# Optimization experiments

Measured on AMD Instinct MI355X. Metric: run time of the kernel, lower is better.

Reference implementation:

```python
import jax, jax.numpy as jnp
import numpy as np

N_HEAD = 16
N_FEAT = 1024
D_K = N_FEAT // N_HEAD  # 64
BLOCK_SIZE = 32
MAX_BLOCKS = 512
CHUNK = 1024
OFFSET = 3072  # cache_seqlens[0]: frames already committed to the cache
SCALE = 0.02


def setup_inputs() -> dict:
    key = jax.random.key(0)
    ks = jax.random.split(key, 12)
    # logical -> physical block mapping: a fixed permutation (irregular access)
    rng = np.random.default_rng(0)
    block_table = jnp.asarray(rng.permutation(MAX_BLOCKS).astype(np.int32))[None, :]
    return {
        "x": jax.random.normal(ks[0], (1, CHUNK, N_FEAT), jnp.float32),
        "Wq": jax.random.normal(ks[1], (N_FEAT, N_FEAT), jnp.float32) * SCALE,
        "bq": jax.random.normal(ks[2], (N_FEAT,), jnp.float32) * SCALE,
        "Wk": jax.random.normal(ks[3], (N_FEAT, N_FEAT), jnp.float32) * SCALE,
        "bk": jax.random.normal(ks[4], (N_FEAT,), jnp.float32) * SCALE,
        "Wv": jax.random.normal(ks[5], (N_FEAT, N_FEAT), jnp.float32) * SCALE,
        "bv": jax.random.normal(ks[6], (N_FEAT,), jnp.float32) * SCALE,
        "Wo": jax.random.normal(ks[7], (N_FEAT, N_FEAT), jnp.float32) * SCALE,
        "bo": jax.random.normal(ks[8], (N_FEAT,), jnp.float32) * SCALE,
        "k_cache": jax.random.normal(ks[9], (MAX_BLOCKS, BLOCK_SIZE, N_HEAD, D_K), jnp.float32),
        "v_cache": jax.random.normal(ks[10], (MAX_BLOCKS, BLOCK_SIZE, N_HEAD, D_K), jnp.float32),
        "block_table": block_table,
        "seqlen_offset": OFFSET,
    }


def reference(x, Wq, bq, Wk, bk, Wv, bv, Wo, bo, k_cache, v_cache, block_table, seqlen_offset):
    B, T, _ = x.shape  # B == 1 (streaming decode)
    # forward_qkv: Q/K/V projections, split into heads
    q = (x @ Wq + bq).reshape(B, T, N_HEAD, D_K).transpose(0, 2, 1, 3)  # (1,h,T,d)
    k_new = (x @ Wk + bk).reshape(B, T, N_HEAD, D_K)                    # (1,T,h,d)
    v_new = (x @ Wv + bv).reshape(B, T, N_HEAD, D_K)

    # _paged_write_kv: scatter the chunk frames into the physical block pool
    pos = seqlen_offset + jnp.arange(T)              # absolute frame indices
    phys = block_table[0, pos // BLOCK_SIZE]         # physical block per frame
    off = pos % BLOCK_SIZE                           # offset within block
    k_cache = k_cache.at[phys, off].set(k_new[0])
    v_cache = v_cache.at[phys, off].set(v_new[0])

    # _paged_gather_kv: gather all total_frames (old + just-written) frames
    total = seqlen_offset + T
    nblk = (total + BLOCK_SIZE - 1) // BLOCK_SIZE
    bids = block_table[0, :nblk]
    kf = k_cache[bids].reshape(-1, N_HEAD, D_K)[:total]  # (total, h, d)
    vf = v_cache[bids].reshape(-1, N_HEAD, D_K)[:total]

    # SDPA over the gathered K/V (no mask; softmax in fp32 as in the source)
    scores = jnp.einsum('bhqd,khd->bhqk', q, kf) / np.float32(np.sqrt(D_K))
    attn = jax.nn.softmax(scores.astype(jnp.float32), axis=-1).astype(x.dtype)
    ctx = jnp.einsum('bhqk,khd->bhqd', attn, vf)         # (1,h,T,d)

    # forward_attention tail: merge heads + output projection
    out = ctx.transpose(0, 2, 1, 3).reshape(B, T, N_HEAD * D_K) @ Wo + bo
    return out
```

## Files before the change

kernel.cpp:

```cpp
#include <hip/hip_runtime.h>
#include <hip/hip_bf16.h>

#define NFEAT 1024
#define NHEAD 16
#define DK 64
#define TCHUNK 1024
#define MAXTOK 4096
#define NSPLIT 4

using bf16x8 = __attribute__((ext_vector_type(8))) short;
using f32x4  = __attribute__((ext_vector_type(4))) float;

__device__ __forceinline__ short f2bf(float f) {
    __hip_bfloat16 h = __float2bfloat16(f);
    return *reinterpret_cast<short*>(&h);
}

__device__ __forceinline__ float exp2fast(float x) {
    return __builtin_amdgcn_exp2f(x);
}

#define QSCALE 0.1803368801f

__global__ __launch_bounds__(256) void pack_kernel(
    const float* __restrict__ x,
    const float* __restrict__ Wq, const float* __restrict__ Wk,
    const float* __restrict__ Wv, const float* __restrict__ Wo,
    short* __restrict__ xb, short* __restrict__ Wt) {
    const int b = blockIdx.x;
    const int t = threadIdx.x;
    if (b < 1024) {
        __shared__ short T[64][72];
        const int w = b >> 8, tile = b & 255;
        const int k0 = (tile >> 4) << 6, n0 = (tile & 15) << 6;
        const float* W = (w == 0) ? Wq : (w == 1) ? Wk : (w == 2) ? Wv : Wo;
        const int r = t >> 2, cs = (t & 3) << 4;
        #pragma unroll
        for (int u = 0; u < 4; ++u) {
            float4 v = *reinterpret_cast<const float4*>(
                &W[(size_t)(k0 + r) * NFEAT + n0 + cs + u * 4]);
            T[cs + u * 4 + 0][r] = f2bf(v.x);
            T[cs + u * 4 + 1][r] = f2bf(v.y);
            T[cs + u * 4 + 2][r] = f2bf(v.z);
            T[cs + u * 4 + 3][r] = f2bf(v.w);
        }
        __syncthreads();
        const int c = t >> 2, rs = (t & 3) << 4;
        bf16x8 a0 = *reinterpret_cast<const bf16x8*>(&T[c][rs]);
        bf16x8 a1 = *reinterpret_cast<const bf16x8*>(&T[c][rs + 8]);
        size_t drow = (size_t)(w * 1024 + n0 + c) * NFEAT + k0 + rs;
        *reinterpret_cast<bf16x8*>(&Wt[drow]) = a0;
        *reinterpret_cast<bf16x8*>(&Wt[drow + 8]) = a1;
    } else {
        const int e0 = ((b - 1024) * 256 + t) * 32;
        #pragma unroll
        for (int u = 0; u < 4; ++u) {
            float4 v0 = *reinterpret_cast<const float4*>(&x[e0 + u * 8]);
            float4 v1 = *reinterpret_cast<const float4*>(&x[e0 + u * 8 + 4]);
            bf16x8 o;
            o[0] = f2bf(v0.x); o[1] = f2bf(v0.y); o[2] = f2bf(v0.z); o[3] = f2bf(v0.w);
            o[4] = f2bf(v1.x); o[5] = f2bf(v1.y); o[6] = f2bf(v1.z); o[7] = f2bf(v1.w);
            *reinterpret_cast<bf16x8*>(&xb[e0 + u * 8]) = o;
        }
    }
}

__global__ __launch_bounds__(256) void qkv_gemm(
    const short* __restrict__ xb, const short* __restrict__ Wt,
    const float* __restrict__ bq, const float* __restrict__ bk,
    const float* __restrict__ bv, short* __restrict__ qkvb) {
    __shared__ short As[64][72];
    __shared__ short Bs[128][72];
    const int tid = threadIdx.x;
    const int lane = tid & 63;
    const int w = tid >> 6;
    const int l15 = lane & 15, lg = lane >> 4;
    const int wr = w >> 1, wc = w & 1;
    const int m0 = blockIdx.y << 6, n0 = blockIdx.x << 7;
    const int sel = n0 >> 10;
    const float* bias = (sel == 0) ? bq : (sel == 1) ? bk : bv;
    const float oscale = (sel == 0) ? QSCALE : 1.0f;

    f32x4 acc[2][4];
    #pragma unroll
    for (int i = 0; i < 2; ++i)
        #pragma unroll
        for (int j = 0; j < 4; ++j) acc[i][j] = (f32x4){0.f, 0.f, 0.f, 0.f};

    for (int k0 = 0; k0 < NFEAT; k0 += 64) {
        #pragma unroll
        for (int r = 0; r < 2; ++r) {
            int f = tid + (r << 8);
            int row = f >> 3, kc = (f & 7) << 3;
            *reinterpret_cast<bf16x8*>(&As[row][kc]) =
                *reinterpret_cast<const bf16x8*>(&xb[(size_t)(m0 + row) * NFEAT + k0 + kc]);
        }
        #pragma unroll
        for (int r = 0; r < 4; ++r) {
            int f = tid + (r << 8);
            int row = f >> 3, kc = (f & 7) << 3;
            *reinterpret_cast<bf16x8*>(&Bs[row][kc]) =
                *reinterpret_cast<const bf16x8*>(&Wt[(size_t)(n0 + row) * NFEAT + k0 + kc]);
        }
        __syncthreads();
        #pragma unroll
        for (int kk = 0; kk < 2; ++kk) {
            bf16x8 am[2], bn[4];
            #pragma unroll
            for (int mi = 0; mi < 2; ++mi)
                am[mi] = *reinterpret_cast<const bf16x8*>(
                    &As[wr * 32 + mi * 16 + l15][kk * 32 + lg * 8]);
            #pragma unroll
            for (int ni = 0; ni < 4; ++ni)
                bn[ni] = *reinterpret_cast<const bf16x8*>(
                    &Bs[wc * 64 + ni * 16 + l15][kk * 32 + lg * 8]);
            #pragma unroll
            for (int mi = 0; mi < 2; ++mi)
                #pragma unroll
                for (int ni = 0; ni < 4; ++ni)
                    acc[mi][ni] = __builtin_amdgcn_mfma_f32_16x16x32_bf16(
                        am[mi], bn[ni], acc[mi][ni], 0, 0, 0);
        }
        __syncthreads();
    }
    #pragma unroll
    for (int mi = 0; mi < 2; ++mi)
        #pragma unroll
        for (int rr = 0; rr < 4; ++rr) {
            int m = m0 + wr * 32 + mi * 16 + lg * 4 + rr;
            #pragma unroll
            for (int ni = 0; ni < 4; ++ni) {
                int n = n0 + wc * 64 + ni * 16 + l15;
                float v = (acc[mi][ni][rr] + bias[n & 1023]) * oscale;
                qkvb[(size_t)m * 3072 + n] = f2bf(v);
            }
        }
}

__global__ __launch_bounds__(256) void out_gemm(
    const short* __restrict__ ctxb, const short* __restrict__ Wt,
    const float* __restrict__ bo, float* __restrict__ out) {
    __shared__ short As[64][72];
    __shared__ short Bs[64][72];
    const int tid = threadIdx.x;
    const int lane = tid & 63;
    const int w = tid >> 6;
    const int l15 = lane & 15, lg = lane >> 4;
    const int wr = w >> 1, wc = w & 1;
    const int m0 = blockIdx.y << 6, n0 = blockIdx.x << 6;

    f32x4 acc[2][2];
    #pragma unroll
    for (int i = 0; i < 2; ++i)
        #pragma unroll
        for (int j = 0; j < 2; ++j) acc[i][j] = (f32x4){0.f, 0.f, 0.f, 0.f};

    for (int k0 = 0; k0 < NFEAT; k0 += 64) {
        #pragma unroll
        for (int r = 0; r < 2; ++r) {
            int f = tid + (r << 8);
            int row = f >> 3, kc = (f & 7) << 3;
            *reinterpret_cast<bf16x8*>(&As[row][kc]) =
                *reinterpret_cast<const bf16x8*>(&ctxb[(size_t)(m0 + row) * NFEAT + k0 + kc]);
            *reinterpret_cast<bf16x8*>(&Bs[row][kc]) =
                *reinterpret_cast<const bf16x8*>(
                    &Wt[(size_t)(3072 + n0 + row) * NFEAT + k0 + kc]);
        }
        __syncthreads();
        #pragma unroll
        for (int kk = 0; kk < 2; ++kk) {
            bf16x8 am[2], bn[2];
            #pragma unroll
            for (int mi = 0; mi < 2; ++mi)
                am[mi] = *reinterpret_cast<const bf16x8*>(
                    &As[wr * 32 + mi * 16 + l15][kk * 32 + lg * 8]);
            #pragma unroll
            for (int ni = 0; ni < 2; ++ni)
                bn[ni] = *reinterpret_cast<const bf16x8*>(
                    &Bs[wc * 32 + ni * 16 + l15][kk * 32 + lg * 8]);
            #pragma unroll
            for (int mi = 0; mi < 2; ++mi)
                #pragma unroll
                for (int ni = 0; ni < 2; ++ni)
                    acc[mi][ni] = __builtin_amdgcn_mfma_f32_16x16x32_bf16(
                        am[mi], bn[ni], acc[mi][ni], 0, 0, 0);
        }
        __syncthreads();
    }
    #pragma unroll
    for (int mi = 0; mi < 2; ++mi)
        #pragma unroll
        for (int rr = 0; rr < 4; ++rr) {
            int m = m0 + wr * 32 + mi * 16 + lg * 4 + rr;
            #pragma unroll
            for (int ni = 0; ni < 2; ++ni) {
                int n = n0 + wc * 32 + ni * 16 + l15;
                out[(size_t)m * NFEAT + n] = acc[mi][ni][rr] + bo[n];
            }
        }
}

__global__ __launch_bounds__(256) void gather_kv(
    const float* __restrict__ kc, const float* __restrict__ vc,
    const short* __restrict__ qkvb, const int* __restrict__ btab,
    const int* __restrict__ soff, short* __restrict__ kg, short* __restrict__ vt) {
    __shared__ short TV[64][72];
    const int h = blockIdx.x;
    const int t0 = blockIdx.y << 6;
    const int offset = soff[0], total = offset + TCHUNK;
    const int t = threadIdx.x;
    const int row = t >> 2, ds = (t & 3) << 4;
    const int tok = t0 + row;
    short kv[16], vv[16];
    if (tok < offset) {
        int phys = btab[tok >> 5];
        size_t base = ((size_t)(phys * 32 + (tok & 31)) * NHEAD + h) * DK + ds;
        #pragma unroll
        for (int u = 0; u < 4; ++u) {
            float4 kf = *reinterpret_cast<const float4*>(&kc[base + u * 4]);
            float4 vf = *reinterpret_cast<const float4*>(&vc[base + u * 4]);
            kv[u * 4 + 0] = f2bf(kf.x); kv[u * 4 + 1] = f2bf(kf.y);
            kv[u * 4 + 2] = f2bf(kf.z); kv[u * 4 + 3] = f2bf(kf.w);
            vv[u * 4 + 0] = f2bf(vf.x); vv[u * 4 + 1] = f2bf(vf.y);
            vv[u * 4 + 2] = f2bf(vf.z); vv[u * 4 + 3] = f2bf(vf.w);
        }
    } else if (tok < total) {
        size_t base = (size_t)(tok - offset) * 3072 + 1024 + h * DK + ds;
        bf16x8 k0 = *reinterpret_cast<const bf16x8*>(&qkvb[base]);
        bf16x8 k1 = *reinterpret_cast<const bf16x8*>(&qkvb[base + 8]);
        bf16x8 v0 = *reinterpret_cast<const bf16x8*>(&qkvb[base + 1024]);
        bf16x8 v1 = *reinterpret_cast<const bf16x8*>(&qkvb[base + 1032]);
        #pragma unroll
        for (int e = 0; e < 8; ++e) {
            kv[e] = k0[e]; kv[8 + e] = k1[e];
            vv[e] = v0[e]; vv[8 + e] = v1[e];
        }
    } else {
        #pragma unroll
        for (int e = 0; e < 16; ++e) { kv[e] = 0; vv[e] = 0; }
    }
    {
        bf16x8 a, b;
        #pragma unroll
        for (int e = 0; e < 8; ++e) { a[e] = kv[e]; b[e] = kv[8 + e]; }
        size_t kb = ((size_t)h * MAXTOK + tok) * DK + ds;
        *reinterpret_cast<bf16x8*>(&kg[kb]) = a;
        *reinterpret_cast<bf16x8*>(&kg[kb + 8]) = b;
    }
    #pragma unroll
    for (int e = 0; e < 16; ++e) TV[ds + e][row] = vv[e];
    __syncthreads();
    {
        const int d = t >> 2, ts = (t & 3) << 4;
        bf16x8 a = *reinterpret_cast<const bf16x8*>(&TV[d][ts]);
        bf16x8 b = *reinterpret_cast<const bf16x8*>(&TV[d][ts + 8]);
        size_t vb = ((size_t)h * DK + d) * MAXTOK + t0 + ts;
        *reinterpret_cast<bf16x8*>(&vt[vb]) = a;
        *reinterpret_cast<bf16x8*>(&vt[vb + 8]) = b;
    }
}

__global__ __launch_bounds__(256, 4) void attn_mfma(
    const short* __restrict__ qkvb, const short* __restrict__ kg,
    const short* __restrict__ vt, const int* __restrict__ soff,
    float* __restrict__ pacc) {
    __shared__ short Ks[64][72];
    __shared__ short Vs[64][72];
    __shared__ short Ps[4][16][72];

    const int tid = threadIdx.x;
    const int lane = tid & 63;
    const int w = tid >> 6;
    const int l15 = lane & 15;
    const int lg = lane >> 4;
    const int h = blockIdx.x;
    const int qt = blockIdx.y;
    const int z = blockIdx.z;
    const int offset = soff[0];
    const int total = offset + TCHUNK;
    const int ntiles = (total + 63) >> 6;
    const int NT = (ntiles + NSPLIT - 1) / NSPLIT;
    const int tbase = z * NT;
    const int tend = min(tbase + NT, ntiles);

    const int srow = tid >> 2;
    const int sds = (tid & 3) << 4;

    const short* kbase = kg + (size_t)h * MAXTOK * DK;
    const short* vbase = vt + (size_t)h * DK * MAXTOK;

    const size_t qrow = (size_t)(qt * 64 + w * 16 + l15) * 3072 + h * DK;
    bf16x8 aq0 = *reinterpret_cast<const bf16x8*>(&qkvb[qrow + lg * 8]);
    bf16x8 aq1 = *reinterpret_cast<const bf16x8*>(&qkvb[qrow + 32 + lg * 8]);

    bf16x8 ones;
    #pragma unroll
    for (int e = 0; e < 8; ++e) ones[e] = (short)0x3F80;

    float m[4];
    f32x4 acc[4], acc1;
    #pragma unroll
    for (int r = 0; r < 4; ++r) m[r] = -1e30f;
    #pragma unroll
    for (int fc = 0; fc < 4; ++fc) acc[fc] = (f32x4){0.f, 0.f, 0.f, 0.f};
    acc1 = (f32x4){0.f, 0.f, 0.f, 0.f};

    bf16x8 kr0, kr1, vr0, vr1;
    if (tbase < tend) {
        int tok0 = tbase << 6;
        size_t kb = (size_t)(tok0 + srow) * DK + sds;
        kr0 = *reinterpret_cast<const bf16x8*>(&kbase[kb]);
        kr1 = *reinterpret_cast<const bf16x8*>(&kbase[kb + 8]);
        size_t vb = (size_t)srow * MAXTOK + tok0 + sds;
        vr0 = *reinterpret_cast<const bf16x8*>(&vbase[vb]);
        vr1 = *reinterpret_cast<const bf16x8*>(&vbase[vb + 8]);
    }

    for (int t = tbase; t < tend; ++t) {
        __syncthreads();
        *reinterpret_cast<bf16x8*>(&Ks[srow][sds]) = kr0;
        *reinterpret_cast<bf16x8*>(&Ks[srow][sds + 8]) = kr1;
        *reinterpret_cast<bf16x8*>(&Vs[srow][sds]) = vr0;
        *reinterpret_cast<bf16x8*>(&Vs[srow][sds + 8]) = vr1;
        __syncthreads();
        if (t + 1 < tend) {
            int tok0 = (t + 1) << 6;
            size_t kb = (size_t)(tok0 + srow) * DK + sds;
            kr0 = *reinterpret_cast<const bf16x8*>(&kbase[kb]);
            kr1 = *reinterpret_cast<const bf16x8*>(&kbase[kb + 8]);
            size_t vb = (size_t)srow * MAXTOK + tok0 + sds;
            vr0 = *reinterpret_cast<const bf16x8*>(&vbase[vb]);
            vr1 = *reinterpret_cast<const bf16x8*>(&vbase[vb + 8]);
        }

        const int kt0 = t << 6;
        bf16x8 kb0[4], kb1[4];
        #pragma unroll
        for (int fc = 0; fc < 4; ++fc) {
            kb0[fc] = *reinterpret_cast<const bf16x8*>(&Ks[fc * 16 + l15][lg * 8]);
            kb1[fc] = *reinterpret_cast<const bf16x8*>(&Ks[fc * 16 + l15][32 + lg * 8]);
        }
        f32x4 s[4];
        __builtin_amdgcn_s_setprio(1);
        #pragma unroll
        for (int fc = 0; fc < 4; ++fc) {
            s[fc] = __builtin_amdgcn_mfma_f32_16x16x32_bf16(
                aq0, kb0[fc], (f32x4){0.f, 0.f, 0.f, 0.f}, 0, 0, 0);
            s[fc] = __builtin_amdgcn_mfma_f32_16x16x32_bf16(
                aq1, kb1[fc], s[fc], 0, 0, 0);
        }
        __builtin_amdgcn_s_setprio(0);
        if (kt0 + 64 > total) {
            #pragma unroll
            for (int fc = 0; fc < 4; ++fc) {
                bool valid = (kt0 + fc * 16 + l15) < total;
                #pragma unroll
                for (int r = 0; r < 4; ++r)
                    s[fc][r] = valid ? s[fc][r] : -1e30f;
            }
        }
        float lm[4];
        #pragma unroll
        for (int r = 0; r < 4; ++r)
            lm[r] = fmaxf(fmaxf(s[0][r], s[1][r]), fmaxf(s[2][r], s[3][r]));
        bool ok = lm[0] <= m[0] + 8.f && lm[1] <= m[1] + 8.f &&
                  lm[2] <= m[2] + 8.f && lm[3] <= m[3] + 8.f;
        if (!__all(ok)) {
            #pragma unroll
            for (int r = 0; r < 4; ++r) {
                float tm = lm[r];
                tm = fmaxf(tm, __shfl_xor(tm, 1));
                tm = fmaxf(tm, __shfl_xor(tm, 2));
                tm = fmaxf(tm, __shfl_xor(tm, 4));
                tm = fmaxf(tm, __shfl_xor(tm, 8));
                float mn = fmaxf(m[r], tm);
                float sc = exp2fast(m[r] - mn);
                m[r] = mn;
                acc1[r] *= sc;
                #pragma unroll
                for (int fc = 0; fc < 4; ++fc) acc[fc][r] *= sc;
            }
        }
        #pragma unroll
        for (int fc = 0; fc < 4; ++fc)
            #pragma unroll
            for (int r = 0; r < 4; ++r)
                Ps[w][lg * 4 + r][l15 + 16 * fc] = f2bf(exp2fast(s[fc][r] - m[r]));
        #pragma unroll
        for (int ks = 0; ks < 2; ++ks) {
            bf16x8 pa = *reinterpret_cast<const bf16x8*>(
                &Ps[w][l15][ks * 32 + lg * 8]);
            __builtin_amdgcn_s_setprio(1);
            acc1 = __builtin_amdgcn_mfma_f32_16x16x32_bf16(pa, ones, acc1, 0, 0, 0);
            #pragma unroll
            for (int fc = 0; fc < 4; ++fc) {
                bf16x8 bv = *reinterpret_cast<const bf16x8*>(
                    &Vs[fc * 16 + l15][ks * 32 + lg * 8]);
                acc[fc] = __builtin_amdgcn_mfma_f32_16x16x32_bf16(pa, bv, acc[fc], 0, 0, 0);
            }
            __builtin_amdgcn_s_setprio(0);
        }
    }

    const size_t pbase = (((size_t)z * NHEAD + h) * 16 + qt) * 4224;
    #pragma unroll
    for (int r = 0; r < 4; ++r) {
        int q = w * 16 + lg * 4 + r;
        if (l15 == 0) {
            pacc[pbase + 4096 + q] = m[r];
            pacc[pbase + 4160 + q] = acc1[r];
        }
        #pragma unroll
        for (int fc = 0; fc < 4; ++fc)
            pacc[pbase + q * 64 + l15 + 16 * fc] = acc[fc][r];
    }
}

__global__ __launch_bounds__(256) void merge_ctx(
    const float* __restrict__ pacc, short* __restrict__ ctxb) {
    const int h = blockIdx.x, qt = blockIdx.y;
    const int t = threadIdx.x;
    const int q = t >> 2, ds = (t & 3) << 4;
    size_t b[NSPLIT];
    float mz[NSPLIT], lz[NSPLIT];
    float M = -1e30f;
    #pragma unroll
    for (int z = 0; z < NSPLIT; ++z) {
        b[z] = (((size_t)z * NHEAD + h) * 16 + qt) * 4224;
        mz[z] = pacc[b[z] + 4096 + q];
        lz[z] = pacc[b[z] + 4160 + q];
        M = fmaxf(M, mz[z]);
    }
    float L = 0.f, ez[NSPLIT];
    #pragma unroll
    for (int z = 0; z < NSPLIT; ++z) {
        ez[z] = __builtin_amdgcn_exp2f(mz[z] - M);
        L += lz[z] * ez[z];
    }
    float inv = 1.f / L;
    bf16x8 o0, o1;
    #pragma unroll
    for (int j = 0; j < 8; ++j) {
        float v = 0.f;
        #pragma unroll
        for (int z = 0; z < NSPLIT; ++z)
            v += pacc[b[z] + q * 64 + ds + j] * ez[z];
        o0[j] = f2bf(v * inv);
    }
    #pragma unroll
    for (int j = 0; j < 8; ++j) {
        float v = 0.f;
        #pragma unroll
        for (int z = 0; z < NSPLIT; ++z)
            v += pacc[b[z] + q * 64 + ds + 8 + j] * ez[z];
        o1[j] = f2bf(v * inv);
    }
    size_t ob = (size_t)(qt * 64 + q) * NFEAT + h * DK + ds;
    *reinterpret_cast<bf16x8*>(&ctxb[ob]) = o0;
    *reinterpret_cast<bf16x8*>(&ctxb[ob + 8]) = o1;
}

extern "C" void kernel_launch(void* const* d_in, const int* in_sizes, int n_in,
                              void* d_out, int out_size, void* d_ws, size_t ws_size,
                              hipStream_t stream) {
    const float* x   = (const float*)d_in[0];
    const float* Wq  = (const float*)d_in[1];
    const float* bq  = (const float*)d_in[2];
    const float* Wk  = (const float*)d_in[3];
    const float* bk  = (const float*)d_in[4];
    const float* Wv  = (const float*)d_in[5];
    const float* bv  = (const float*)d_in[6];
    const float* Wo  = (const float*)d_in[7];
    const float* bo  = (const float*)d_in[8];
    const float* kc  = (const float*)d_in[9];
    const float* vc  = (const float*)d_in[10];
    const int*   bt  = (const int*)d_in[11];
    const int*   so  = (const int*)d_in[12];

    short* xb   = (short*)d_ws;
    short* Wt   = xb + (size_t)1024 * 1024;
    short* qkvb = Wt + (size_t)4096 * 1024;
    short* kg   = qkvb + (size_t)1024 * 3072;
    short* vtb  = kg + (size_t)NHEAD * MAXTOK * DK;
    float* pacc = (float*)(vtb + (size_t)NHEAD * DK * MAXTOK);
    short* ctxb = (short*)(pacc + (size_t)NSPLIT * 256 * 4224);

    pack_kernel<<<dim3(1152), 256, 0, stream>>>(x, Wq, Wk, Wv, Wo, xb, Wt);
    qkv_gemm<<<dim3(24, 16), 256, 0, stream>>>(xb, Wt, bq, bk, bv, qkvb);
    gather_kv<<<dim3(16, 64), 256, 0, stream>>>(kc, vc, qkvb, bt, so, kg, vtb);
    attn_mfma<<<dim3(16, 16, NSPLIT), 256, 0, stream>>>(qkvb, kg, vtb, so, pacc);
    merge_ctx<<<dim3(16, 16), 256, 0, stream>>>(pacc, ctxb);
    out_gemm<<<dim3(16, 16), 256, 0, stream>>>(ctxb, Wt, bo, (float*)d_out);
}
```

Before: 105.2 us.

## Load K/V MFMA operands directly from global memory, drop LDS staging, split six ways

Removes the shared-memory staging of K and V tiles, along with the two block-wide barriers per tile and the register prefetch. Each wave now reads its MFMA B-operands straight from global memory. The KV split rises from 4 to 6 and the occupancy hint from 4 to 6 blocks per CU, so more blocks are in flight. Every wave now fetches the full K/V tile itself, which means 4x redundant global/L2 traffic, and there is no longer explicit prefetch to hide load latency.

```diff
diff --git a/kernel.cpp b/kernel.cpp
--- a/kernel.cpp
+++ b/kernel.cpp
@@ -6,7 +6,7 @@
 #define DK 64
 #define TCHUNK 1024
 #define MAXTOK 4096
-#define NSPLIT 4
+#define NSPLIT 6
 
 using bf16x8 = __attribute__((ext_vector_type(8))) short;
 using f32x4  = __attribute__((ext_vector_type(4))) float;
@@ -260,12 +260,10 @@
     }
 }
 
-__global__ __launch_bounds__(256, 4) void attn_mfma(
+__global__ __launch_bounds__(256, 6) void attn_mfma(
     const short* __restrict__ qkvb, const short* __restrict__ kg,
     const short* __restrict__ vt, const int* __restrict__ soff,
     float* __restrict__ pacc) {
-    __shared__ short Ks[64][72];
-    __shared__ short Vs[64][72];
     __shared__ short Ps[4][16][72];
 
     const int tid = threadIdx.x;
@@ -283,9 +281,6 @@
     const int tbase = z * NT;
     const int tend = min(tbase + NT, ntiles);
 
-    const int srow = tid >> 2;
-    const int sds = (tid & 3) << 4;
-
     const short* kbase = kg + (size_t)h * MAXTOK * DK;
     const short* vbase = vt + (size_t)h * DK * MAXTOK;
 
@@ -305,40 +300,14 @@
     for (int fc = 0; fc < 4; ++fc) acc[fc] = (f32x4){0.f, 0.f, 0.f, 0.f};
     acc1 = (f32x4){0.f, 0.f, 0.f, 0.f};
 
-    bf16x8 kr0, kr1, vr0, vr1;
-    if (tbase < tend) {
-        int tok0 = tbase << 6;
-        size_t kb = (size_t)(tok0 + srow) * DK + sds;
-        kr0 = *reinterpret_cast<const bf16x8*>(&kbase[kb]);
-        kr1 = *reinterpret_cast<const bf16x8*>(&kbase[kb + 8]);
-        size_t vb = (size_t)srow * MAXTOK + tok0 + sds;
-        vr0 = *reinterpret_cast<const bf16x8*>(&vbase[vb]);
-        vr1 = *reinterpret_cast<const bf16x8*>(&vbase[vb + 8]);
-    }
-
     for (int t = tbase; t < tend; ++t) {
-        __syncthreads();
-        *reinterpret_cast<bf16x8*>(&Ks[srow][sds]) = kr0;
-        *reinterpret_cast<bf16x8*>(&Ks[srow][sds + 8]) = kr1;
-        *reinterpret_cast<bf16x8*>(&Vs[srow][sds]) = vr0;
-        *reinterpret_cast<bf16x8*>(&Vs[srow][sds + 8]) = vr1;
-        __syncthreads();
-        if (t + 1 < tend) {
-            int tok0 = (t + 1) << 6;
-            size_t kb = (size_t)(tok0 + srow) * DK + sds;
-            kr0 = *reinterpret_cast<const bf16x8*>(&kbase[kb]);
-            kr1 = *reinterpret_cast<const bf16x8*>(&kbase[kb + 8]);
-            size_t vb = (size_t)srow * MAXTOK + tok0 + sds;
-            vr0 = *reinterpret_cast<const bf16x8*>(&vbase[vb]);
-            vr1 = *reinterpret_cast<const bf16x8*>(&vbase[vb + 8]);
-        }
-
         const int kt0 = t << 6;
         bf16x8 kb0[4], kb1[4];
         #pragma unroll
         for (int fc = 0; fc < 4; ++fc) {
-            kb0[fc] = *reinterpret_cast<const bf16x8*>(&Ks[fc * 16 + l15][lg * 8]);
-            kb1[fc] = *reinterpret_cast<const bf16x8*>(&Ks[fc * 16 + l15][32 + lg * 8]);
+            size_t kb = (size_t)(kt0 + fc * 16 + l15) * DK + lg * 8;
+            kb0[fc] = *reinterpret_cast<const bf16x8*>(&kbase[kb]);
+            kb1[fc] = *reinterpret_cast<const bf16x8*>(&kbase[kb + 32]);
         }
         f32x4 s[4];
         __builtin_amdgcn_s_setprio(1);
@@ -395,7 +364,7 @@
             #pragma unroll
             for (int fc = 0; fc < 4; ++fc) {
                 bf16x8 bv = *reinterpret_cast<const bf16x8*>(
-                    &Vs[fc * 16 + l15][ks * 32 + lg * 8]);
+                    &vbase[(size_t)(fc * 16 + l15) * MAXTOK + kt0 + ks * 32 + lg * 8]);
                 acc[fc] = __builtin_amdgcn_mfma_f32_16x16x32_bf16(pa, bv, acc[fc], 0, 0, 0);
             }
             __builtin_amdgcn_s_setprio(0);
```

Result: slower. 228.4 us (+117.1%).
